# Kernel tuning notes

Measured on AMD Instinct MI355X. Metric: run time of the kernel, lower is better.

## Reference

```python
import jax, jax.numpy as jnp
import numpy as np

BETA = 0.25
N_E = 8192
E_DIM = 512


def setup_inputs() -> dict:
    key = jax.random.key(0)
    k1, k2 = jax.random.split(key)
    z = jax.random.normal(k1, (16, 2048, E_DIM), dtype=jnp.float32)
    mask = jnp.ones((16, 2048), dtype=jnp.float32)
    # torch init: uniform(-1/n_e, 1/n_e)
    emb = jax.random.uniform(k2, (N_E, E_DIM), dtype=jnp.float32,
                             minval=-1.0 / N_E, maxval=1.0 / N_E)
    return {"z": z, "mask": mask, "emb": emb}


def reference(z, mask, emb):
    B, S, H = z.shape
    z_flat = z.reshape(-1, H)  # (B*S, H)
    # squared L2 distances to every codebook entry: (B*S, n_e)
    d = (jnp.sum(z_flat ** 2, axis=1, keepdims=True)
         + jnp.sum(emb ** 2, axis=1)
         - 2.0 * jnp.matmul(z_flat, emb.T))
    idx = jnp.argmin(d, axis=1)  # (B*S,)
    # gather codebook rows (equivalent to one-hot @ emb, without materializing one-hot)
    z_q = emb[idx].reshape(z.shape)
    m = mask[..., None]  # (B, S, 1)
    sg = jax.lax.stop_gradient
    loss = (jnp.mean((sg(z_q) - z) ** 2 * m)
            + BETA * jnp.mean((z_q - sg(z)) ** 2 * m))
    # straight-through estimator
    z_q_st = z + sg(z_q - z)
    return z_q_st, idx[:, None], loss
```

## Files before the change

kernel.cpp:

```cpp
#include <hip/hip_runtime.h>

#define N_E 8192
#define E_DIM 512
#define NROWS 32768
#define TOT_ELEMS 16777216
#define BETA 0.25f

#define GBM 128
#define GBN 256
#define GBK 64
#define NGROUPS 64
#define MARGIN 3.0e-4f

typedef __attribute__((ext_vector_type(8))) short short8v;
typedef __attribute__((ext_vector_type(4))) float f32x4;

#define GLD16(gp, lp)                                                          \
    __builtin_amdgcn_global_load_lds(                                          \
        (const __attribute__((address_space(1))) void*)(gp),                   \
        (__attribute__((address_space(3))) void*)(lp), 16, 0, 0)

__device__ __forceinline__ unsigned short f2bf(float f) {
    unsigned u = __float_as_uint(f);
    u += 0x7FFFu + ((u >> 16) & 1u);
    return (unsigned short)(u >> 16);
}
__device__ __forceinline__ unsigned long long packwi(float w, int col) {
    return ((unsigned long long)__float_as_uint(w) << 32) | (unsigned)col;
}
__device__ __forceinline__ float valof(unsigned long long p) {
    return __uint_as_float((unsigned)(p >> 32));
}

__global__ __launch_bounds__(256) void z2_kernel(const float* __restrict__ z,
                                                 float* __restrict__ z2,
                                                 unsigned long long* __restrict__ zb8) {
    int row  = blockIdx.x * 4 + (threadIdx.x >> 6);
    int lane = threadIdx.x & 63;
    const float4* p = (const float4*)(z + (size_t)row * E_DIM);
    double s = 0.0;
#pragma unroll
    for (int it = 0; it < 2; ++it) {
        float4 v = p[lane + it * 64];
        s += (double)v.x * v.x + (double)v.y * v.y
           + (double)v.z * v.z + (double)v.w * v.w;
        unsigned long long pk =
              (unsigned long long)((unsigned)f2bf(v.x) | ((unsigned)f2bf(v.y) << 16))
            | ((unsigned long long)((unsigned)f2bf(v.z) | ((unsigned)f2bf(v.w) << 16)) << 32);
        zb8[(size_t)row * 128 + lane + it * 64] = pk;
    }
#pragma unroll
    for (int off = 32; off > 0; off >>= 1) s += __shfl_down(s, off);
    if (lane == 0) z2[row] = (float)s;
}

__global__ __launch_bounds__(256) void convb_kernel(const float* __restrict__ emb,
                                                    unsigned long long* __restrict__ embb8) {
    int t = blockIdx.x * 256 + threadIdx.x;
    float4 v = ((const float4*)emb)[t];
    unsigned long long p =
          (unsigned long long)((unsigned)f2bf(v.x) | ((unsigned)f2bf(v.y) << 16))
        | ((unsigned long long)((unsigned)f2bf(v.z) | ((unsigned)f2bf(v.w) << 16)) << 32);
    embb8[t] = p;
}

__global__ __launch_bounds__(512) void gemm_argmin_kernel(
        const unsigned short* __restrict__ zb,
        const unsigned short* __restrict__ embb,
        const float* __restrict__ z2s,
        unsigned long long* __restrict__ m1g) {
    __shared__ __align__(16) char smem[GBM * GBK * 2 + GBN * GBK * 2];
    unsigned short* Al = (unsigned short*)smem;
    unsigned short* Bl = (unsigned short*)(smem + GBM * GBK * 2);
    __shared__ float z2sh[GBM];

    const int tid  = threadIdx.x;
    const int lane = tid & 63;
    const int wid  = tid >> 6;
    const int wr   = wid >> 2;
    const int wc   = wid & 3;
    const int bx   = blockIdx.x & 31;
    const int by   = blockIdx.x >> 5;
    const int row0 = by * GBM;
    const int nb0  = bx * GBN;

    if (tid < GBM) z2sh[tid] = z2s[row0 + tid];

    const int lrow = lane >> 3;
    const int lswz = ((lane & 7) ^ (lrow & 7)) * 8;
    const unsigned short* srcA0 = zb + (size_t)(row0 + wid * 16 + lrow) * E_DIM + lswz;
    const unsigned short* srcA1 = srcA0 + 8 * E_DIM;
    unsigned short* dstA0 = Al + (wid * 2) * 512;
    unsigned short* dstA1 = dstA0 + 512;
    const unsigned short* srcB0 = embb + (size_t)(nb0 + wid * 32 + lrow) * E_DIM + lswz;
    const unsigned short* srcB1 = srcB0 + 8 * E_DIM;
    const unsigned short* srcB2 = srcB0 + 16 * E_DIM;
    const unsigned short* srcB3 = srcB0 + 24 * E_DIM;
    unsigned short* dstB0 = Bl + (wid * 4) * 512;
    unsigned short* dstB1 = dstB0 + 512;
    unsigned short* dstB2 = dstB0 + 1024;
    unsigned short* dstB3 = dstB0 + 1536;

    int aoff[4], boff[4];
#pragma unroll
    for (int ri = 0; ri < 4; ++ri) {
        int rowf = wr * 64 + ri * 16 + (lane & 15);
        aoff[ri] = rowf * 128 + (((lane >> 4) ^ (rowf & 7)) << 4);
    }
#pragma unroll
    for (int ci = 0; ci < 4; ++ci) {
        int rowf = wc * 64 + ci * 16 + (lane & 15);
        boff[ci] = rowf * 128 + (((lane >> 4) ^ (rowf & 7)) << 4);
    }

    f32x4 acc[4][4];
#pragma unroll
    for (int a = 0; a < 4; ++a)
#pragma unroll
        for (int b = 0; b < 4; ++b) acc[a][b] = (f32x4){0.f, 0.f, 0.f, 0.f};

#pragma unroll
    for (int kt = 0; kt < 8; ++kt) {
        GLD16(srcA0 + kt * GBK, dstA0);
        GLD16(srcA1 + kt * GBK, dstA1);
        GLD16(srcB0 + kt * GBK, dstB0);
        GLD16(srcB1 + kt * GBK, dstB1);
        GLD16(srcB2 + kt * GBK, dstB2);
        GLD16(srcB3 + kt * GBK, dstB3);
        __syncthreads();

#pragma unroll
        for (int kh = 0; kh < 2; ++kh) {
            short8v af[4], bfr[4];
#pragma unroll
            for (int ri = 0; ri < 4; ++ri)
                af[ri] = *(const short8v*)((const char*)Al + (aoff[ri] ^ (kh << 6)));
#pragma unroll
            for (int ci = 0; ci < 4; ++ci)
                bfr[ci] = *(const short8v*)((const char*)Bl + (boff[ci] ^ (kh << 6)));
#pragma unroll
            for (int ri = 0; ri < 4; ++ri)
#pragma unroll
                for (int ci = 0; ci < 4; ++ci)
                    acc[ri][ci] = __builtin_amdgcn_mfma_f32_16x16x32_bf16(
                        af[ri], bfr[ci], acc[ri][ci], 0, 0, 0);
        }
        __syncthreads();
    }

    unsigned long long* m1L = (unsigned long long*)smem;
    float*              m2L = (float*)(smem + 4096);
    const int colb = nb0 + wc * 64 + (lane & 15);
#pragma unroll
    for (int ri = 0; ri < 4; ++ri) {
#pragma unroll
        for (int i = 0; i < 4; ++i) {
            int row = wr * 64 + ri * 16 + ((lane >> 4) << 2) + i;
            float z2r = z2sh[row];
            float w0 = z2r - 2.f * acc[ri][0][i];
            float w1 = z2r - 2.f * acc[ri][1][i];
            float w2 = z2r - 2.f * acc[ri][2][i];
            float w3 = z2r - 2.f * acc[ri][3][i];
            unsigned long long m1 = packwi(w0, colb);
            float m2 = 3.4e38f;
            unsigned long long p;
            p = packwi(w1, colb + 16);
            if (p < m1) { m2 = valof(m1); m1 = p; } else m2 = fminf(m2, w1);
            p = packwi(w2, colb + 32);
            if (p < m1) { m2 = valof(m1); m1 = p; } else m2 = fminf(m2, w2);
            p = packwi(w3, colb + 48);
            if (p < m1) { m2 = valof(m1); m1 = p; } else m2 = fminf(m2, w3);
#pragma unroll
            for (int off = 1; off < 16; off <<= 1) {
                unsigned long long o1 = __shfl_xor(m1, off);
                float o2 = __shfl_xor(m2, off);
                float hi = fmaxf(valof(m1), valof(o1));
                m2 = fminf(fminf(m2, o2), hi);
                if (o1 < m1) m1 = o1;
            }
            if ((lane & 15) == ri * 4 + i) {
                m1L[row * 4 + wc] = m1;
                m2L[row * 4 + wc] = m2;
            }
        }
    }
    __syncthreads();

    if (tid < 256) {
        int row = tid >> 1, h = tid & 1;
        unsigned long long a = m1L[row * 4 + 2 * h];
        unsigned long long b = m1L[row * 4 + 2 * h + 1];
        float ma = m2L[row * 4 + 2 * h];
        float mb = m2L[row * 4 + 2 * h + 1];
        unsigned long long m1c = a < b ? a : b;
        float m2c = fminf(fminf(ma, mb), fmaxf(valof(a), valof(b)));
        float wv  = valof(m1c);
        unsigned col = (unsigned)(m1c & 0xFFFFu);
        unsigned dl  = __float_as_uint(m2c - wv) >> 16;
        unsigned long long packed =
              ((unsigned long long)__float_as_uint(wv) << 32)
            | ((unsigned long long)col << 16) | dl;
        m1g[(size_t)(row0 + row) * NGROUPS + bx * 2 + h] = packed;
    }
}

__device__ __forceinline__ float exact_w(const float* zs, const float* __restrict__ emb,
                                         int col, float z2r) {
    const float* e = emb + (size_t)col * E_DIM;
    float acc = 0.f;
#pragma unroll 8
    for (int k = 0; k < E_DIM; ++k) acc = fmaf(zs[k], e[k], acc);
    return z2r - 2.f * acc;
}

__global__ __launch_bounds__(256) void rescore_kernel(
        const float* __restrict__ z, const float* __restrict__ emb,
        const float* __restrict__ z2s,
        const unsigned long long* __restrict__ m1g,
        float* __restrict__ idxf) {
    __shared__ __align__(16) float zsh[4][512];
    const int lane = threadIdx.x & 63;
    const int wid  = threadIdx.x >> 6;
    const int r    = blockIdx.x * 4 + wid;

    const float4* zr4 = (const float4*)(z + (size_t)r * E_DIM);
    ((float4*)zsh[wid])[lane]      = zr4[lane];
    ((float4*)zsh[wid])[lane + 64] = zr4[lane + 64];
    __syncthreads();
    const float* zs  = zsh[wid];
    const float  z2r = z2s[r];

    unsigned long long e = m1g[(size_t)r * NGROUPS + lane];
    float w1  = __uint_as_float((unsigned)(e >> 32));
    int   c1  = (int)((e >> 16) & 0xFFFFu);
    float dlb = __uint_as_float(((unsigned)e & 0xFFFFu) << 16);

    float gm = w1;
#pragma unroll
    for (int off = 1; off < 64; off <<= 1)
        gm = fminf(gm, __shfl_xor(gm, off));
    const float thr = gm + MARGIN;

    float wb = 3.4e38f; int ib = 0x7fffffff;
    if (w1 <= thr) {
        float w = exact_w(zs, emb, c1, z2r);
        if (w < wb || (w == wb && c1 < ib)) { wb = w; ib = c1; }
    }
    unsigned long long mf = __ballot(w1 + dlb <= thr);
    while (mf) {
        int g = __ffsll((long long)mf) - 1; mf &= mf - 1;
        int col = g * 128 + lane;
        float w = exact_w(zs, emb, col, z2r);
        if (w < wb || (w == wb && col < ib)) { wb = w; ib = col; }
        col += 64;
        w = exact_w(zs, emb, col, z2r);
        if (w < wb || (w == wb && col < ib)) { wb = w; ib = col; }
    }
#pragma unroll
    for (int off = 1; off < 64; off <<= 1) {
        float wo = __shfl_xor(wb, off);
        int  io  = __shfl_xor(ib, off);
        if (wo < wb || (wo == wb && io < ib)) { wb = wo; ib = io; }
    }
    if (lane == 0) idxf[r] = (float)ib;
}

__global__ __launch_bounds__(256) void output_kernel(const float* __restrict__ z,
                                                     const float* __restrict__ mask,
                                                     const float* __restrict__ emb,
                                                     const float* __restrict__ idxf,
                                                     float* __restrict__ out0,
                                                     float* __restrict__ loss) {
    const int nth = gridDim.x * blockDim.x;
    int t = blockIdx.x * blockDim.x + threadIdx.x;
    const float4* z4 = (const float4*)z;
    const float4* e4 = (const float4*)emb;
    float4* o4 = (float4*)out0;
    float partial = 0.f;
    for (int f = t; f < TOT_ELEMS / 4; f += nth) {
        int row = f >> 7;
        int col = f & 127;
        int id  = (int)idxf[row];
        float m = mask[row];
        float4 zv = z4[f];
        float4 qv = e4[id * 128 + col];
        float dx = qv.x - zv.x, dy = qv.y - zv.y;
        float dz = qv.z - zv.z, dw = qv.w - zv.w;
        float4 ov;
        ov.x = zv.x + dx; ov.y = zv.y + dy;
        ov.z = zv.z + dz; ov.w = zv.w + dw;
        o4[f] = ov;
        partial += (dx * dx + dy * dy + dz * dz + dw * dw) * m;
    }
#pragma unroll
    for (int off = 32; off > 0; off >>= 1) partial += __shfl_down(partial, off);
    __shared__ float wsum[4];
    int lane = threadIdx.x & 63, w = threadIdx.x >> 6;
    if (lane == 0) wsum[w] = partial;
    __syncthreads();
    if (threadIdx.x == 0) {
        float s = wsum[0] + wsum[1] + wsum[2] + wsum[3];
        atomicAdd(loss, s * ((1.f + BETA) / (float)TOT_ELEMS));
    }
}

extern "C" void kernel_launch(void* const* d_in, const int* in_sizes, int n_in,
                              void* d_out, int out_size, void* d_ws, size_t ws_size,
                              hipStream_t stream) {
    const float* z    = (const float*)d_in[0];
    const float* mask = (const float*)d_in[1];
    const float* emb  = (const float*)d_in[2];

    float* out0 = (float*)d_out;
    float* out1 = out0 + TOT_ELEMS;
    float* loss = out1 + NROWS;

    char* base = (char*)d_out;
    unsigned long long* m1g  = (unsigned long long*)base;
    unsigned short*     zb   = (unsigned short*)(base + 16777216);
    unsigned short*     embb = (unsigned short*)(base + 50331648);
    float*              z2st = (float*)(base + 58720256);

    hipMemsetAsync(loss, 0, sizeof(float), stream);
    z2_kernel<<<NROWS / 4, 256, 0, stream>>>(z, z2st, (unsigned long long*)zb);
    convb_kernel<<<4096, 256, 0, stream>>>(emb, (unsigned long long*)embb);
    gemm_argmin_kernel<<<(NROWS / GBM) * (N_E / GBN), 512, 0, stream>>>(
        zb, embb, z2st, m1g);
    rescore_kernel<<<NROWS / 4, 256, 0, stream>>>(z, emb, z2st, m1g, out1);
    output_kernel<<<4096, 256, 0, stream>>>(z, mask, emb, out1, out0, loss);
}
```

Measured before the change: 862.6 us.

## Split GEMM block tile across 16 waves with 32x64 per-wave subtiles

Doubles the GEMM-argmin block from 512 to 1024 threads while keeping the same 128x256 block tile. Each wave now computes a 32x64 subtile instead of 64x64, and the LDS staging and swizzle are rewritten for one A load and two B loads per thread. The aim is more waves per CU for latency hiding and fewer accumulator registers per wave. The cost is fewer MFMAs per LDS fragment read. The launch bounds of (1024, 4) may also squeeze VGPRs hard enough to cause spills.

```diff
diff --git a/kernel.cpp b/kernel.cpp
--- a/kernel.cpp
+++ b/kernel.cpp
@@ -64,7 +64,7 @@
     embb8[t] = p;
 }
 
-__global__ __launch_bounds__(512) void gemm_argmin_kernel(
+__global__ __launch_bounds__(1024, 4) void gemm_argmin_kernel(
         const unsigned short* __restrict__ zb,
         const unsigned short* __restrict__ embb,
         const float* __restrict__ z2s,
@@ -87,63 +87,51 @@
     if (tid < GBM) z2sh[tid] = z2s[row0 + tid];
 
     const int lrow = lane >> 3;
-    const int lswz = ((lane & 7) ^ (lrow & 7)) * 8;
-    const unsigned short* srcA0 = zb + (size_t)(row0 + wid * 16 + lrow) * E_DIM + lswz;
-    const unsigned short* srcA1 = srcA0 + 8 * E_DIM;
-    unsigned short* dstA0 = Al + (wid * 2) * 512;
-    unsigned short* dstA1 = dstA0 + 512;
-    const unsigned short* srcB0 = embb + (size_t)(nb0 + wid * 32 + lrow) * E_DIM + lswz;
+    const int lswz = ((lane & 7) ^ lrow) * 8;
+    const unsigned short* srcA  = zb   + (size_t)(row0 + wid * 8  + lrow) * E_DIM + lswz;
+    const unsigned short* srcB0 = embb + (size_t)(nb0 + wid * 16 + lrow) * E_DIM + lswz;
     const unsigned short* srcB1 = srcB0 + 8 * E_DIM;
-    const unsigned short* srcB2 = srcB0 + 16 * E_DIM;
-    const unsigned short* srcB3 = srcB0 + 24 * E_DIM;
-    unsigned short* dstB0 = Bl + (wid * 4) * 512;
+    unsigned short* dstA  = Al + wid * 512;
+    unsigned short* dstB0 = Bl + wid * 1024;
     unsigned short* dstB1 = dstB0 + 512;
-    unsigned short* dstB2 = dstB0 + 1024;
-    unsigned short* dstB3 = dstB0 + 1536;
-
-    int aoff[4], boff[4];
-#pragma unroll
-    for (int ri = 0; ri < 4; ++ri) {
-        int rowf = wr * 64 + ri * 16 + (lane & 15);
-        aoff[ri] = rowf * 128 + (((lane >> 4) ^ (rowf & 7)) << 4);
-    }
-#pragma unroll
-    for (int ci = 0; ci < 4; ++ci) {
-        int rowf = wc * 64 + ci * 16 + (lane & 15);
-        boff[ci] = rowf * 128 + (((lane >> 4) ^ (rowf & 7)) << 4);
-    }
-
-    f32x4 acc[4][4];
-#pragma unroll
-    for (int a = 0; a < 4; ++a)
+
+    const int swz = ((lane >> 4) ^ (lane & 7)) << 4;
+    const int aof  = (wr * 32 + (lane & 15)) * 128 + swz;
+    const int bof  = (wc * 64 + (lane & 15)) * 128 + swz;
+    const int aof1 = aof ^ 64;
+    const int bof1 = bof ^ 64;
+
+    f32x4 acc[2][4];
+#pragma unroll
+    for (int a = 0; a < 2; ++a)
 #pragma unroll
         for (int b = 0; b < 4; ++b) acc[a][b] = (f32x4){0.f, 0.f, 0.f, 0.f};
 
 #pragma unroll
     for (int kt = 0; kt < 8; ++kt) {
-        GLD16(srcA0 + kt * GBK, dstA0);
-        GLD16(srcA1 + kt * GBK, dstA1);
+        GLD16(srcA  + kt * GBK, dstA);
         GLD16(srcB0 + kt * GBK, dstB0);
         GLD16(srcB1 + kt * GBK, dstB1);
-        GLD16(srcB2 + kt * GBK, dstB2);
-        GLD16(srcB3 + kt * GBK, dstB3);
         __syncthreads();
 
 #pragma unroll
         for (int kh = 0; kh < 2; ++kh) {
-            short8v af[4], bfr[4];
-#pragma unroll
-            for (int ri = 0; ri < 4; ++ri)
-                af[ri] = *(const short8v*)((const char*)Al + (aoff[ri] ^ (kh << 6)));
-#pragma unroll
-            for (int ci = 0; ci < 4; ++ci)
-                bfr[ci] = *(const short8v*)((const char*)Bl + (boff[ci] ^ (kh << 6)));
-#pragma unroll
-            for (int ri = 0; ri < 4; ++ri)
-#pragma unroll
-                for (int ci = 0; ci < 4; ++ci)
-                    acc[ri][ci] = __builtin_amdgcn_mfma_f32_16x16x32_bf16(
-                        af[ri], bfr[ci], acc[ri][ci], 0, 0, 0);
+            const int ak = kh ? aof1 : aof;
+            const int bk = kh ? bof1 : bof;
+            short8v a0 = *(const short8v*)((const char*)Al + ak);
+            short8v a1 = *(const short8v*)((const char*)Al + ak + 2048);
+            short8v b0 = *(const short8v*)((const char*)Bl + bk);
+            short8v b1 = *(const short8v*)((const char*)Bl + bk + 2048);
+            short8v b2 = *(const short8v*)((const char*)Bl + bk + 4096);
+            short8v b3 = *(const short8v*)((const char*)Bl + bk + 6144);
+            acc[0][0] = __builtin_amdgcn_mfma_f32_16x16x32_bf16(a0, b0, acc[0][0], 0, 0, 0);
+            acc[0][1] = __builtin_amdgcn_mfma_f32_16x16x32_bf16(a0, b1, acc[0][1], 0, 0, 0);
+            acc[0][2] = __builtin_amdgcn_mfma_f32_16x16x32_bf16(a0, b2, acc[0][2], 0, 0, 0);
+            acc[0][3] = __builtin_amdgcn_mfma_f32_16x16x32_bf16(a0, b3, acc[0][3], 0, 0, 0);
+            acc[1][0] = __builtin_amdgcn_mfma_f32_16x16x32_bf16(a1, b0, acc[1][0], 0, 0, 0);
+            acc[1][1] = __builtin_amdgcn_mfma_f32_16x16x32_bf16(a1, b1, acc[1][1], 0, 0, 0);
+            acc[1][2] = __builtin_amdgcn_mfma_f32_16x16x32_bf16(a1, b2, acc[1][2], 0, 0, 0);
+            acc[1][3] = __builtin_amdgcn_mfma_f32_16x16x32_bf16(a1, b3, acc[1][3], 0, 0, 0);
         }
         __syncthreads();
     }
@@ -152,10 +140,10 @@
     float*              m2L = (float*)(smem + 4096);
     const int colb = nb0 + wc * 64 + (lane & 15);
 #pragma unroll
-    for (int ri = 0; ri < 4; ++ri) {
+    for (int ri = 0; ri < 2; ++ri) {
 #pragma unroll
         for (int i = 0; i < 4; ++i) {
-            int row = wr * 64 + ri * 16 + ((lane >> 4) << 2) + i;
+            int row = wr * 32 + ri * 16 + ((lane >> 4) << 2) + i;
             float z2r = z2sh[row];
             float w0 = z2r - 2.f * acc[ri][0][i];
             float w1 = z2r - 2.f * acc[ri][1][i];
@@ -324,7 +312,7 @@
     hipMemsetAsync(loss, 0, sizeof(float), stream);
     z2_kernel<<<NROWS / 4, 256, 0, stream>>>(z, z2st, (unsigned long long*)zb);
     convb_kernel<<<4096, 256, 0, stream>>>(emb, (unsigned long long*)embb);
-    gemm_argmin_kernel<<<(NROWS / GBM) * (N_E / GBN), 512, 0, stream>>>(
+    gemm_argmin_kernel<<<(NROWS / GBM) * (N_E / GBN), 1024, 0, stream>>>(
         zb, embb, z2st, m1g);
     rescore_kernel<<<NROWS / 4, 256, 0, stream>>>(z, emb, z2st, m1g, out1);
     output_kernel<<<4096, 256, 0, stream>>>(z, mask, emb, out1, out0, loss);
```

New measurement: 848.1 us. About the same (-1.7%).
